# Optimization experiments

Hardware: AMD Instinct MI355X
Metric: run time of the kernel (lower is better)

The kernel has to match this reference:

```python
import jax, jax.numpy as jnp
import numpy as np

B, V, C, H, W, D = 1, 3, 64, 96, 96, 48


def bilinear_sample(feat, gx, gy):
    """torch F.grid_sample(mode='bilinear', padding_mode='zeros', align_corners=True).
    feat: (B, C, H, W); gx, gy: (B, N) normalized coords in [-1, 1]. Returns (B, C, N)."""
    Bf, Cf, Hf, Wf = feat.shape
    x = (gx + 1.0) * 0.5 * (Wf - 1)
    y = (gy + 1.0) * 0.5 * (Hf - 1)
    x0 = jnp.floor(x)
    y0 = jnp.floor(y)
    wx1 = x - x0
    wy1 = y - y0
    wx0 = 1.0 - wx1
    wy0 = 1.0 - wy1
    flat = feat.reshape(Bf, Cf, Hf * Wf)

    def gather(xi, yi):
        valid = (xi >= 0) & (xi <= Wf - 1) & (yi >= 0) & (yi <= Hf - 1)
        xi_c = jnp.clip(xi, 0, Wf - 1).astype(jnp.int32)
        yi_c = jnp.clip(yi, 0, Hf - 1).astype(jnp.int32)
        idx = (yi_c * Wf + xi_c)[:, None, :]  # (B,1,N), broadcast over C
        return jnp.take_along_axis(flat, idx, axis=2) * valid[:, None, :]

    out = (gather(x0, y0) * (wx0 * wy0)[:, None]
           + gather(x0 + 1, y0) * (wx1 * wy0)[:, None]
           + gather(x0, y0 + 1) * (wx0 * wy1)[:, None]
           + gather(x0 + 1, y0 + 1) * (wx1 * wy1)[:, None])
    return out


def src_grid(proj_mat, depth_values, Hs, Ws):
    """homo_warp grid computation. proj_mat: (B,3,4); depth_values: (B,D).
    Returns normalized gx, gy each of shape (B, D*Hs*Ws)."""
    xs = jnp.arange(Ws, dtype=jnp.float32)
    ys = jnp.arange(Hs, dtype=jnp.float32)
    gx_, gy_ = jnp.meshgrid(xs, ys)  # (Hs, Ws) each
    ref = jnp.stack([gx_.ravel(), gy_.ravel(), jnp.ones(Hs * Ws, jnp.float32)], 0)  # (3, HW)
    R = proj_mat[:, :, :3]
    T = proj_mat[:, :, 3]
    # (B,3,D,HW): R @ p + T / depth
    pts = jnp.einsum('bij,jn->bin', R, ref)[:, :, None, :] + T[:, :, None, None] / depth_values[:, None, :, None]
    xy = pts[:, :2] / pts[:, 2:3]
    gx = xy[:, 0] / ((Ws - 1) / 2.0) - 1.0
    gy = xy[:, 1] / ((Hs - 1) / 2.0) - 1.0
    Bb = proj_mat.shape[0]
    return gx.reshape(Bb, -1), gy.reshape(Bb, -1)


def setup_inputs() -> dict:
    key = jax.random.key(0)
    k1, k2, k3, k4 = jax.random.split(key, 4)
    imgs = jax.random.normal(k1, (B, V, 3, H, W), jnp.float32)
    feats = jax.random.normal(k2, (B, V, C, H, W), jnp.float32)
    # near-identity projections so warped coords land mostly in-range (z ~ 1)
    eye = jnp.broadcast_to(jnp.eye(3, dtype=jnp.float32), (B, V, 3, 3))
    Rn = eye + 0.05 * jax.random.normal(k3, (B, V, 3, 3), jnp.float32)
    Tn = 0.5 * jax.random.normal(jax.random.fold_in(k3, 1), (B, V, 3, 1), jnp.float32)
    proj_mats = jnp.concatenate([Rn, Tn], axis=-1)
    depth_values = 2.0 + 4.0 * jax.random.uniform(k4, (B, D), jnp.float32)
    return {"imgs": imgs, "feats": feats, "proj_mats": proj_mats, "depth_values": depth_values}


def reference(imgs, feats, proj_mats, depth_values):
    Bb, Vv, _, Hh, Ww = imgs.shape
    Cc = feats.shape[2]
    Dd = depth_values.shape[1]
    # ref view volume (broadcast over D)
    ref_volume = jnp.broadcast_to(feats[:, 0][:, :, None], (Bb, Cc, Dd, Hh, Ww))
    volume_sum = ref_volume
    volume_sq_sum = ref_volume ** 2
    mask_sum = jnp.ones((Bb, Dd, Hh, Ww), jnp.float32)  # ref view always in-range
    img_chans = [jnp.broadcast_to(imgs[:, 0][:, :, None], (Bb, 3, Dd, Hh, Ww))]
    for i in range(Vv - 1):  # small fixed number of source views
        gx, gy = src_grid(proj_mats[:, i + 1], depth_values, Hh, Ww)
        wv = bilinear_sample(feats[:, i + 1], gx, gy).reshape(Bb, Cc, Dd, Hh, Ww)
        wi = bilinear_sample(imgs[:, i + 1], gx, gy).reshape(Bb, 3, Dd, Hh, Ww)
        m = ((gx > -1.0) & (gx < 1.0) & (gy > -1.0) & (gy < 1.0)).astype(jnp.float32).reshape(Bb, Dd, Hh, Ww)
        volume_sum = volume_sum + wv
        volume_sq_sum = volume_sq_sum + wv ** 2
        mask_sum = mask_sum + m
        img_chans.append(wi)
    count = 1.0 / mask_sum[:, None]  # (B,1,D,H,W)
    var = volume_sq_sum * count - (volume_sum * count) ** 2  # (B,C,D,H,W)
    img_chans.append(var)
    return jnp.concatenate(img_chans, axis=1)  # (B, 3*V + C, D, H, W)
```

## Files before the change

kernel.cpp:

```cpp
#include <hip/hip_runtime.h>

#define BDIM 256

constexpr int Vv = 3, Cc = 64, Hh = 96, Ww = 96, Dd = 48;
constexpr int HW = Hh * Ww;
constexpr int NPIX = Dd * HW;
constexpr int DHW = Dd * HW;

__device__ __forceinline__ void compute_warp(const float* __restrict__ proj, float depth,
                                             float xf, float yf,
                                             int offs[2][4], float wts[2][4], float& msum)
{
    msum = 1.0f;
#pragma unroll
    for (int v = 0; v < 2; ++v) {
#pragma clang fp contract(off)
        const float* P = proj + (v + 1) * 12;
        const float r00 = P[0], r01 = P[1], r02 = P[2],  t0 = P[3];
        const float r10 = P[4], r11 = P[5], r12 = P[6],  t1 = P[7];
        const float r20 = P[8], r21 = P[9], r22 = P[10], t2 = P[11];

        const float px = ((r00 * xf + r01 * yf) + r02) + t0 / depth;
        const float py = ((r10 * xf + r11 * yf) + r12) + t1 / depth;
        const float pz = ((r20 * xf + r21 * yf) + r22) + t2 / depth;

        const float xy0 = px / pz;
        const float xy1 = py / pz;
        const float gx = xy0 / ((float)(Ww - 1) * 0.5f) - 1.0f;
        const float gy = xy1 / ((float)(Hh - 1) * 0.5f) - 1.0f;

        const bool inb = (gx > -1.0f) && (gx < 1.0f) && (gy > -1.0f) && (gy < 1.0f);
        msum += inb ? 1.0f : 0.0f;

        const float sx = (gx + 1.0f) * 0.5f * (float)(Ww - 1);
        const float sy = (gy + 1.0f) * 0.5f * (float)(Hh - 1);
        const float x0 = floorf(sx), y0 = floorf(sy);
        const float wx1 = sx - x0, wy1 = sy - y0;
        const float wx0 = 1.0f - wx1, wy0 = 1.0f - wy1;

#pragma unroll
        for (int k = 0; k < 4; ++k) {
            const float xi = (k & 1) ? (x0 + 1.0f) : x0;
            const float yi = (k & 2) ? (y0 + 1.0f) : y0;
            const float wk = ((k & 1) ? wx1 : wx0) * ((k & 2) ? wy1 : wy0);
            const bool valid = (xi >= 0.0f) && (xi <= (float)(Ww - 1)) &&
                               (yi >= 0.0f) && (yi <= (float)(Hh - 1));
            const float xc = fminf(fmaxf(xi, 0.0f), (float)(Ww - 1));
            const float yc = fminf(fmaxf(yi, 0.0f), (float)(Hh - 1));
            offs[v][k] = (int)yc * Ww + (int)xc;
            wts[v][k] = valid ? wk : 0.0f;
        }
    }
}

__global__ void __launch_bounds__(BDIM) transpose_feats_kernel(const float* __restrict__ feats,
                                                               float* __restrict__ ft)
{
    __shared__ float tile[64][65];
    const int v  = blockIdx.y;
    const int p0 = blockIdx.x * 64;
    const float* src = feats + (size_t)v * Cc * HW;

    const int px = threadIdx.x & 63;
    const int c0 = threadIdx.x >> 6;
#pragma unroll
    for (int c = c0; c < Cc; c += 4)
        tile[c][px] = src[(size_t)c * HW + p0 + px];
    __syncthreads();

    const int cc  = threadIdx.x & 63;
    const int pr0 = threadIdx.x >> 6;
    float* dst = ft + ((size_t)v * HW + p0) * Cc;
#pragma unroll
    for (int p = pr0; p < 64; p += 4)
        dst[p * Cc + cc] = tile[cc][p];
}

__global__ void __launch_bounds__(BDIM) transpose_imgs_kernel(const float* __restrict__ imgs,
                                                              float* __restrict__ it)
{
    const int idx = blockIdx.x * BDIM + threadIdx.x;
    if (idx >= 2 * HW) return;
    const int v = idx / HW;
    const int p = idx - v * HW;
    const float* src = imgs + (size_t)(v + 1) * 3 * HW + p;
    float4 o;
    o.x = src[0];
    o.y = src[HW];
    o.z = src[2 * HW];
    o.w = 0.0f;
    ((float4*)it)[idx] = o;
}

__global__ void __launch_bounds__(BDIM, 4) ge_main_kernel(
    const float* __restrict__ imgs, const float* __restrict__ ftr,
    const float* __restrict__ it, const float* __restrict__ proj,
    const float* __restrict__ depthv, float* __restrict__ out)
{
    const int idx = blockIdx.x * BDIM + threadIdx.x;
    if (idx >= NPIX) return;
    const int w = idx % Ww;
    const int t = idx / Ww;
    const int h = t % Hh;
    const int d = t / Hh;
    const int ohw = h * Ww + w;

    int offs[2][4];
    float wts[2][4];
    float msum;
    compute_warp(proj, depthv[d], (float)w, (float)h, offs, wts, msum);

    const int obase = d * HW + ohw;

#pragma unroll
    for (int c = 0; c < 3; ++c)
        out[c * DHW + obase] = imgs[c * HW + ohw];

    const float4* itv = (const float4*)it;
#pragma unroll
    for (int v = 0; v < 2; ++v) {
        const float4 p0 = itv[(size_t)v * HW + offs[v][0]];
        const float4 p1 = itv[(size_t)v * HW + offs[v][1]];
        const float4 p2 = itv[(size_t)v * HW + offs[v][2]];
        const float4 p3 = itv[(size_t)v * HW + offs[v][3]];
        const float w0 = wts[v][0], w1 = wts[v][1], w2 = wts[v][2], w3 = wts[v][3];
        out[(3 * (v + 1) + 0) * DHW + obase] = w0 * p0.x + w1 * p1.x + w2 * p2.x + w3 * p3.x;
        out[(3 * (v + 1) + 1) * DHW + obase] = w0 * p0.y + w1 * p1.y + w2 * p2.y + w3 * p3.y;
        out[(3 * (v + 1) + 2) * DHW + obase] = w0 * p0.z + w1 * p1.z + w2 * p2.z + w3 * p3.z;
    }

    const float count = 1.0f / msum;
    const float4* f0  = (const float4*)ftr + (size_t)ohw * 16;
    const float4* c10 = (const float4*)ftr + ((size_t)HW + offs[0][0]) * 16;
    const float4* c11 = (const float4*)ftr + ((size_t)HW + offs[0][1]) * 16;
    const float4* c12 = (const float4*)ftr + ((size_t)HW + offs[0][2]) * 16;
    const float4* c13 = (const float4*)ftr + ((size_t)HW + offs[0][3]) * 16;
    const float4* c20 = (const float4*)ftr + ((size_t)2 * HW + offs[1][0]) * 16;
    const float4* c21 = (const float4*)ftr + ((size_t)2 * HW + offs[1][1]) * 16;
    const float4* c22 = (const float4*)ftr + ((size_t)2 * HW + offs[1][2]) * 16;
    const float4* c23 = (const float4*)ftr + ((size_t)2 * HW + offs[1][3]) * 16;
    const float w00 = wts[0][0], w01 = wts[0][1], w02 = wts[0][2], w03 = wts[0][3];
    const float w10 = wts[1][0], w11 = wts[1][1], w12 = wts[1][2], w13 = wts[1][3];
    float* ob = out + 9 * DHW + obase;

#define VARCOMP(comp, cidx)                                                     \
    do {                                                                        \
        const float A_ = w00 * a0.comp + w01 * a1.comp + w02 * a2.comp + w03 * a3.comp; \
        const float B_ = w10 * b0.comp + w11 * b1.comp + w12 * b2.comp + w13 * b3.comp; \
        const float S_ = fr.comp + A_ + B_;                                     \
        const float Q_ = fr.comp * fr.comp + A_ * A_ + B_ * B_;                 \
        const float sc_ = S_ * count;                                           \
        ob[(size_t)(4 * j + (cidx)) * DHW] = Q_ * count - sc_ * sc_;            \
    } while (0)

#pragma unroll 4
    for (int j = 0; j < 16; ++j) {
        const float4 fr = f0[j];
        const float4 a0 = c10[j], a1 = c11[j], a2 = c12[j], a3 = c13[j];
        const float4 b0 = c20[j], b1 = c21[j], b2 = c22[j], b3 = c23[j];
        VARCOMP(x, 0);
        VARCOMP(y, 1);
        VARCOMP(z, 2);
        VARCOMP(w, 3);
    }
#undef VARCOMP
}

__global__ void __launch_bounds__(BDIM) ge_direct_kernel(
    const float* __restrict__ imgs, const float* __restrict__ feats,
    const float* __restrict__ proj, const float* __restrict__ depthv,
    float* __restrict__ out)
{
    const int idx = blockIdx.x * BDIM + threadIdx.x;
    if (idx >= NPIX) return;
    const int w = idx % Ww;
    const int t = idx / Ww;
    const int h = t % Hh;
    const int d = t / Hh;
    const int ohw = h * Ww + w;

    int offs[2][4];
    float wts[2][4];
    float msum;
    compute_warp(proj, depthv[d], (float)w, (float)h, offs, wts, msum);

    const int obase = d * HW + ohw;
#pragma unroll
    for (int c = 0; c < 3; ++c)
        out[c * DHW + obase] = imgs[c * HW + ohw];

#pragma unroll
    for (int v = 0; v < 2; ++v) {
        const float* ib = imgs + (size_t)(v + 1) * 3 * HW;
#pragma unroll
        for (int c = 0; c < 3; ++c) {
            const float* p = ib + (size_t)c * HW;
            const float acc = wts[v][0] * p[offs[v][0]] + wts[v][1] * p[offs[v][1]] +
                              wts[v][2] * p[offs[v][2]] + wts[v][3] * p[offs[v][3]];
            out[(3 * (v + 1) + c) * DHW + obase] = acc;
        }
    }

    const float count = 1.0f / msum;
    const float* f0 = feats;
    const float* f1 = feats + (size_t)Cc * HW;
    const float* f2 = feats + (size_t)2 * Cc * HW;
#pragma unroll 8
    for (int c = 0; c < Cc; ++c) {
        const float fr = f0[(size_t)c * HW + ohw];
        const float* p1 = f1 + (size_t)c * HW;
        const float* p2 = f2 + (size_t)c * HW;
        const float a1 = wts[0][0] * p1[offs[0][0]] + wts[0][1] * p1[offs[0][1]] +
                         wts[0][2] * p1[offs[0][2]] + wts[0][3] * p1[offs[0][3]];
        const float a2 = wts[1][0] * p2[offs[1][0]] + wts[1][1] * p2[offs[1][1]] +
                         wts[1][2] * p2[offs[1][2]] + wts[1][3] * p2[offs[1][3]];
        const float s = fr + a1 + a2;
        const float sq = fr * fr + a1 * a1 + a2 * a2;
        const float sc = s * count;
        out[(3 * Vv + c) * DHW + obase] = sq * count - sc * sc;
    }
}

extern "C" void kernel_launch(void* const* d_in, const int* in_sizes, int n_in,
                              void* d_out, int out_size, void* d_ws, size_t ws_size,
                              hipStream_t stream)
{
    const float* imgs   = (const float*)d_in[0];
    const float* feats  = (const float*)d_in[1];
    const float* proj   = (const float*)d_in[2];
    const float* depthv = (const float*)d_in[3];
    float* out = (float*)d_out;

    const size_t need = (size_t)Vv * HW * Cc * sizeof(float)
                      + (size_t)2 * HW * 4 * sizeof(float);
    const int blocks = (NPIX + BDIM - 1) / BDIM;

    if (ws_size >= need) {
        float* ftr = (float*)d_ws;
        float* it  = ftr + (size_t)Vv * HW * Cc;
        dim3 g1(HW / 64, Vv);
        transpose_feats_kernel<<<g1, BDIM, 0, stream>>>(feats, ftr);
        transpose_imgs_kernel<<<(2 * HW + BDIM - 1) / BDIM, BDIM, 0, stream>>>(imgs, it);
        ge_main_kernel<<<blocks, BDIM, 0, stream>>>(imgs, ftr, it, proj, depthv, out);
    } else {
        ge_direct_kernel<<<blocks, BDIM, 0, stream>>>(imgs, feats, proj, depthv, out);
    }
}
```

Before: 209.8 us.

## Process one output row per block with channel-parallel gathers and LDS-staged stores

```diff
diff --git a/kernel.cpp b/kernel.cpp
--- a/kernel.cpp
+++ b/kernel.cpp
@@ -76,94 +76,92 @@
         dst[p * Cc + cc] = tile[cc][p];
 }
 
-__global__ void __launch_bounds__(BDIM) transpose_imgs_kernel(const float* __restrict__ imgs,
-                                                              float* __restrict__ it)
-{
-    const int idx = blockIdx.x * BDIM + threadIdx.x;
-    if (idx >= 2 * HW) return;
-    const int v = idx / HW;
-    const int p = idx - v * HW;
-    const float* src = imgs + (size_t)(v + 1) * 3 * HW + p;
-    float4 o;
-    o.x = src[0];
-    o.y = src[HW];
-    o.z = src[2 * HW];
-    o.w = 0.0f;
-    ((float4*)it)[idx] = o;
-}
-
-__global__ void __launch_bounds__(BDIM, 4) ge_main_kernel(
+__global__ void __launch_bounds__(BDIM) ge_row_kernel(
     const float* __restrict__ imgs, const float* __restrict__ ftr,
-    const float* __restrict__ it, const float* __restrict__ proj,
-    const float* __restrict__ depthv, float* __restrict__ out)
-{
-    const int idx = blockIdx.x * BDIM + threadIdx.x;
-    if (idx >= NPIX) return;
-    const int w = idx % Ww;
-    const int t = idx / Ww;
-    const int h = t % Hh;
-    const int d = t / Hh;
-    const int ohw = h * Ww + w;
-
-    int offs[2][4];
-    float wts[2][4];
-    float msum;
-    compute_warp(proj, depthv[d], (float)w, (float)h, offs, wts, msum);
-
-    const int obase = d * HW + ohw;
-
-#pragma unroll
-    for (int c = 0; c < 3; ++c)
-        out[c * DHW + obase] = imgs[c * HW + ohw];
-
-    const float4* itv = (const float4*)it;
-#pragma unroll
-    for (int v = 0; v < 2; ++v) {
-        const float4 p0 = itv[(size_t)v * HW + offs[v][0]];
-        const float4 p1 = itv[(size_t)v * HW + offs[v][1]];
-        const float4 p2 = itv[(size_t)v * HW + offs[v][2]];
-        const float4 p3 = itv[(size_t)v * HW + offs[v][3]];
-        const float w0 = wts[v][0], w1 = wts[v][1], w2 = wts[v][2], w3 = wts[v][3];
-        out[(3 * (v + 1) + 0) * DHW + obase] = w0 * p0.x + w1 * p1.x + w2 * p2.x + w3 * p3.x;
-        out[(3 * (v + 1) + 1) * DHW + obase] = w0 * p0.y + w1 * p1.y + w2 * p2.y + w3 * p3.y;
-        out[(3 * (v + 1) + 2) * DHW + obase] = w0 * p0.z + w1 * p1.z + w2 * p2.z + w3 * p3.z;
-    }
-
-    const float count = 1.0f / msum;
-    const float4* f0  = (const float4*)ftr + (size_t)ohw * 16;
-    const float4* c10 = (const float4*)ftr + ((size_t)HW + offs[0][0]) * 16;
-    const float4* c11 = (const float4*)ftr + ((size_t)HW + offs[0][1]) * 16;
-    const float4* c12 = (const float4*)ftr + ((size_t)HW + offs[0][2]) * 16;
-    const float4* c13 = (const float4*)ftr + ((size_t)HW + offs[0][3]) * 16;
-    const float4* c20 = (const float4*)ftr + ((size_t)2 * HW + offs[1][0]) * 16;
-    const float4* c21 = (const float4*)ftr + ((size_t)2 * HW + offs[1][1]) * 16;
-    const float4* c22 = (const float4*)ftr + ((size_t)2 * HW + offs[1][2]) * 16;
-    const float4* c23 = (const float4*)ftr + ((size_t)2 * HW + offs[1][3]) * 16;
-    const float w00 = wts[0][0], w01 = wts[0][1], w02 = wts[0][2], w03 = wts[0][3];
-    const float w10 = wts[1][0], w11 = wts[1][1], w12 = wts[1][2], w13 = wts[1][3];
-    float* ob = out + 9 * DHW + obase;
-
-#define VARCOMP(comp, cidx)                                                     \
-    do {                                                                        \
-        const float A_ = w00 * a0.comp + w01 * a1.comp + w02 * a2.comp + w03 * a3.comp; \
-        const float B_ = w10 * b0.comp + w11 * b1.comp + w12 * b2.comp + w13 * b3.comp; \
-        const float S_ = fr.comp + A_ + B_;                                     \
-        const float Q_ = fr.comp * fr.comp + A_ * A_ + B_ * B_;                 \
-        const float sc_ = S_ * count;                                           \
-        ob[(size_t)(4 * j + (cidx)) * DHW] = Q_ * count - sc_ * sc_;            \
-    } while (0)
-
-#pragma unroll 4
-    for (int j = 0; j < 16; ++j) {
-        const float4 fr = f0[j];
-        const float4 a0 = c10[j], a1 = c11[j], a2 = c12[j], a3 = c13[j];
-        const float4 b0 = c20[j], b1 = c21[j], b2 = c22[j], b3 = c23[j];
-        VARCOMP(x, 0);
-        VARCOMP(y, 1);
-        VARCOMP(z, 2);
-        VARCOMP(w, 3);
-    }
-#undef VARCOMP
+    const float* __restrict__ proj, const float* __restrict__ depthv,
+    float* __restrict__ out)
+{
+    __shared__ float s_tile[Cc][Ww + 1];
+    __shared__ int   s_base[2][4][Ww];
+    __shared__ float s_wt[2][4][Ww];
+    __shared__ float s_cnt[Ww];
+
+    const int blk = blockIdx.x;
+    const int d   = blk / Hh;
+    const int h   = blk % Hh;
+    const int tid = threadIdx.x;
+    const int rowbase = d * HW + h * Ww;
+
+    if (tid < Ww) {
+        const int w = tid;
+        int offs[2][4];
+        float wts[2][4];
+        float msum;
+        compute_warp(proj, depthv[d], (float)w, (float)h, offs, wts, msum);
+        s_cnt[w] = 1.0f / msum;
+#pragma unroll
+        for (int v = 0; v < 2; ++v)
+#pragma unroll
+            for (int k = 0; k < 4; ++k) {
+                s_base[v][k][w] = ((v + 1) * HW + offs[v][k]) * Cc;
+                s_wt[v][k][w]   = wts[v][k];
+            }
+
+        const int hw = h * Ww + w;
+#pragma unroll
+        for (int c = 0; c < 3; ++c)
+            out[c * DHW + rowbase + w] = imgs[c * HW + hw];
+
+#pragma unroll
+        for (int v = 0; v < 2; ++v) {
+            const float* ib = imgs + (size_t)(v + 1) * 3 * HW;
+#pragma unroll
+            for (int c = 0; c < 3; ++c) {
+                const float* p = ib + (size_t)c * HW;
+                const float acc = wts[v][0] * p[offs[v][0]] + wts[v][1] * p[offs[v][1]] +
+                                  wts[v][2] * p[offs[v][2]] + wts[v][3] * p[offs[v][3]];
+                out[(3 * (v + 1) + c) * DHW + rowbase + w] = acc;
+            }
+        }
+    }
+    __syncthreads();
+
+    {
+        const int wave = tid >> 6;
+        const int c    = tid & 63;
+        const int p0   = wave * (Ww / 4);
+#pragma unroll 2
+        for (int i = 0; i < Ww / 4; ++i) {
+            const int p = p0 + i;
+            const float cnt = s_cnt[p];
+            const int b00 = s_base[0][0][p], b01 = s_base[0][1][p];
+            const int b02 = s_base[0][2][p], b03 = s_base[0][3][p];
+            const int b10 = s_base[1][0][p], b11 = s_base[1][1][p];
+            const int b12 = s_base[1][2][p], b13 = s_base[1][3][p];
+            const float w00 = s_wt[0][0][p], w01 = s_wt[0][1][p];
+            const float w02 = s_wt[0][2][p], w03 = s_wt[0][3][p];
+            const float w10 = s_wt[1][0][p], w11 = s_wt[1][1][p];
+            const float w12 = s_wt[1][2][p], w13 = s_wt[1][3][p];
+
+            const float fr = ftr[(size_t)(h * Ww + p) * Cc + c];
+            const float a1 = w00 * ftr[b00 + c] + w01 * ftr[b01 + c] +
+                             w02 * ftr[b02 + c] + w03 * ftr[b03 + c];
+            const float a2 = w10 * ftr[b10 + c] + w11 * ftr[b11 + c] +
+                             w12 * ftr[b12 + c] + w13 * ftr[b13 + c];
+            const float s  = fr + a1 + a2;
+            const float q  = fr * fr + a1 * a1 + a2 * a2;
+            const float sc = s * cnt;
+            s_tile[c][p] = q * cnt - sc * sc;
+        }
+    }
+    __syncthreads();
+
+#pragma unroll
+    for (int idx = tid; idx < Cc * Ww; idx += BDIM) {
+        const int cc = idx / Ww;
+        const int p  = idx - cc * Ww;
+        out[(9 + cc) * DHW + rowbase + p] = s_tile[cc][p];
+    }
 }
 
 __global__ void __launch_bounds__(BDIM) ge_direct_kernel(
@@ -231,18 +229,15 @@
     const float* depthv = (const float*)d_in[3];
     float* out = (float*)d_out;
 
-    const size_t need = (size_t)Vv * HW * Cc * sizeof(float)
-                      + (size_t)2 * HW * 4 * sizeof(float);
-    const int blocks = (NPIX + BDIM - 1) / BDIM;
+    const size_t need = (size_t)Vv * HW * Cc * sizeof(float);
 
     if (ws_size >= need) {
         float* ftr = (float*)d_ws;
-        float* it  = ftr + (size_t)Vv * HW * Cc;
         dim3 g1(HW / 64, Vv);
         transpose_feats_kernel<<<g1, BDIM, 0, stream>>>(feats, ftr);
-        transpose_imgs_kernel<<<(2 * HW + BDIM - 1) / BDIM, BDIM, 0, stream>>>(imgs, it);
-        ge_main_kernel<<<blocks, BDIM, 0, stream>>>(imgs, ftr, it, proj, depthv, out);
+        ge_row_kernel<<<Dd * Hh, BDIM, 0, stream>>>(imgs, ftr, proj, depthv, out);
     } else {
+        const int blocks = (NPIX + BDIM - 1) / BDIM;
         ge_direct_kernel<<<blocks, BDIM, 0, stream>>>(imgs, feats, proj, depthv, out);
     }
 }
```

New measurement: 180.6 us. 13.9% less time.
